# Kernel optimization log

Hardware: AMD Instinct MI355X
Metric: run time of the kernel (lower is better)

Reference implementation:

```python
import jax, jax.numpy as jnp
import numpy as np

EMBED_DIM = 768
N_HEADS = 12
HEAD_DIM = EMBED_DIM // N_HEADS


def setup_inputs() -> dict:
    key = jax.random.key(0)
    ks = jax.random.split(key, 6)
    bsz, seq = 2, 4096
    hidden_states = jax.random.normal(ks[0], (bsz, seq, EMBED_DIM), dtype=jnp.float32)
    attention_mask = jnp.zeros((bsz, 1, 1, seq), dtype=jnp.float32)
    s = 1.0 / np.sqrt(EMBED_DIM)
    Wq = jax.random.normal(ks[1], (EMBED_DIM, EMBED_DIM), dtype=jnp.float32) * s
    Wk = jax.random.normal(ks[2], (EMBED_DIM, EMBED_DIM), dtype=jnp.float32) * s
    Wv = jax.random.normal(ks[3], (EMBED_DIM, EMBED_DIM), dtype=jnp.float32) * s
    Wo = jax.random.normal(ks[4], (EMBED_DIM, EMBED_DIM), dtype=jnp.float32) * s
    bo = jax.random.normal(ks[5], (EMBED_DIM,), dtype=jnp.float32) * s
    return {"hidden_states": hidden_states, "attention_mask": attention_mask,
            "Wq": Wq, "Wk": Wk, "Wv": Wv, "Wo": Wo, "bo": bo}


def reference(hidden_states, attention_mask, Wq, Wk, Wv, Wo, bo):
    bsz, seq, _ = hidden_states.shape
    scale = 1.0 / np.sqrt(HEAD_DIM)

    def split_heads(x):  # [b, s, e] -> [b, h, s, d]
        return x.reshape(bsz, seq, N_HEADS, HEAD_DIM).transpose(0, 2, 1, 3)

    # nn.Linear applies x @ W.T
    q = split_heads(hidden_states @ Wq.T)
    k = split_heads(hidden_states @ Wk.T)
    v = split_heads(hidden_states @ Wv.T)

    # [b, h, tgt, src] score matrix (faithful to the bmm+softmax+bmm original)
    attn = jnp.einsum('bhqd,bhkd->bhqk', q, k) * scale
    attn = attn + attention_mask  # mask broadcasts [b,1,1,src]
    probs = jax.nn.softmax(attn, axis=-1)
    ctx = jnp.einsum('bhqk,bhkd->bhqd', probs, v)

    concat = ctx.transpose(0, 2, 1, 3).reshape(bsz, seq, EMBED_DIM)
    return concat @ Wo.T + bo
```

## Files before the change

kernel.cpp:

```cpp
#include <hip/hip_runtime.h>
#include <stdint.h>

#define ED   768
#define NH   12
#define HD   64
#define SEQ  4096
#define BSZ  2
#define BHT  (BSZ*NH)
#define MTOT (BSZ*SEQ)

typedef short bf16x8  __attribute__((ext_vector_type(8)));
typedef float f32x4   __attribute__((ext_vector_type(4)));
typedef float f32x16  __attribute__((ext_vector_type(16)));

#define LOG2E 1.44269504088896340736f
#define C2    (0.125f * LOG2E)

__device__ __forceinline__ unsigned short f2bf(float f) {
    union { float f; uint32_t u; } v; v.f = f;
    uint32_t u = v.u;
    u += 0x7fffu + ((u >> 16) & 1u);
    return (unsigned short)(u >> 16);
}

#if defined(__has_builtin)
#if __has_builtin(__builtin_amdgcn_cvt_pk_bf16_f32)
#define HAVE_CVT_PK_BF16 1
#endif
#endif
__device__ __forceinline__ uint32_t pkbf16(float a, float b) {
#ifdef HAVE_CVT_PK_BF16
    typedef __bf16 bf16x2_t __attribute__((ext_vector_type(2)));
    union { bf16x2_t v; uint32_t u; } c;
    c.v = __builtin_amdgcn_cvt_pk_bf16_f32(a, b);
    return c.u;
#else
    union { float f; uint32_t u; } x, y; x.f = a; y.f = b;
    return __builtin_amdgcn_perm(y.u + 0x8000u, x.u + 0x8000u, 0x07060302u);
#endif
}

__device__ __forceinline__ void cp16(const unsigned short* g, unsigned short* l) {
    __builtin_amdgcn_global_load_lds(
        (const __attribute__((address_space(1))) unsigned int*)(const void*)g,
        (__attribute__((address_space(3))) unsigned int*)(void*)l,
        16, 0, 0);
}

#define H_CHUNKS  (MTOT * ED / 4)
#define W_CHUNKS  (ED * ED / 4)
#define CVT_TOTAL (H_CHUNKS + 4 * W_CHUNKS)

__global__ __launch_bounds__(256) void convert_bf16(
    const float* __restrict__ H,  const float* __restrict__ Wq,
    const float* __restrict__ Wk, const float* __restrict__ Wv,
    const float* __restrict__ Wo, unsigned short* __restrict__ dst,
    unsigned short* __restrict__ WoB) {
    int i4 = blockIdx.x * 256 + threadIdx.x;
    float4 v;
    ushort4* optr;
    if (i4 < H_CHUNKS) { v = ((const float4*)H)[i4]; optr = (ushort4*)dst + i4; }
    else {
        int j = i4 - H_CHUNKS;
        if (j < 3 * W_CHUNKS) {
            if (j < W_CHUNKS)          v = ((const float4*)Wq)[j];
            else if (j < 2 * W_CHUNKS) v = ((const float4*)Wk)[j - W_CHUNKS];
            else                       v = ((const float4*)Wv)[j - 2 * W_CHUNKS];
            optr = (ushort4*)dst + i4;
        } else {
            v = ((const float4*)Wo)[j - 3 * W_CHUNKS];
            optr = (ushort4*)WoB + (j - 3 * W_CHUNKS);
        }
    }
    ushort4 o;
    o.x = f2bf(v.x); o.y = f2bf(v.y); o.z = f2bf(v.z); o.w = f2bf(v.w);
    *optr = o;
}

__global__ __launch_bounds__(256) void qkv_gemm(
    const unsigned short* __restrict__ Hb,
    const unsigned short* __restrict__ Wb,
    unsigned short* __restrict__ qkv) {
    __shared__ __align__(16) unsigned short Ah[128 * 64];
    __shared__ __align__(16) unsigned short Bh[128 * 64];
    const int t = threadIdx.x, w = t >> 6, lane = t & 63;
    const int quad = lane >> 4, r16 = lane & 15;
    const int wm = w >> 1, wn = w & 1;
    const int m0 = blockIdx.y * 128, n0g = blockIdx.x * 128;
    const int wsel = n0g / ED, n0 = n0g % ED;
    const int lrow = lane >> 3;
    const int lchs = ((lane & 7) ^ (lrow & 7)) * 8;

    f32x4 acc[4][4] = {};
    for (int kt = 0; kt < ED / 64; ++kt) {
        const int k0 = kt * 64;
#pragma unroll
        for (int i = 0; i < 4; ++i) {
            int row = i * 32 + w * 8;
            cp16(&Hb[(size_t)(m0 + row + lrow) * ED + k0 + lchs], &Ah[row * 64]);
            cp16(&Wb[(size_t)(n0g + row + lrow) * ED + k0 + lchs], &Bh[row * 64]);
        }
        __syncthreads();
#pragma unroll
        for (int kk = 0; kk < 2; ++kk) {
            bf16x8 aF[4], bF[4];
#pragma unroll
            for (int mi = 0; mi < 4; ++mi) {
                int R = wm * 64 + mi * 16 + r16;
                aF[mi] = *(const bf16x8*)&Ah[R * 64 + (((kk * 4 + quad) ^ (r16 & 7)) * 8)];
            }
#pragma unroll
            for (int ni = 0; ni < 4; ++ni) {
                int R = wn * 64 + ni * 16 + r16;
                bF[ni] = *(const bf16x8*)&Bh[R * 64 + (((kk * 4 + quad) ^ (r16 & 7)) * 8)];
            }
            if (wsel == 2) {
#pragma unroll
                for (int mi = 0; mi < 4; ++mi)
#pragma unroll
                    for (int ni = 0; ni < 4; ++ni)
                        acc[mi][ni] = __builtin_amdgcn_mfma_f32_16x16x32_bf16(
                            bF[ni], aF[mi], acc[mi][ni], 0, 0, 0);
            } else {
#pragma unroll
                for (int mi = 0; mi < 4; ++mi)
#pragma unroll
                    for (int ni = 0; ni < 4; ++ni)
                        acc[mi][ni] = __builtin_amdgcn_mfma_f32_16x16x32_bf16(
                            aF[mi], bF[ni], acc[mi][ni], 0, 0, 0);
            }
        }
        __syncthreads();
    }
    const size_t WSZ = (size_t)BHT * SEQ * HD;
    if (wsel == 2) {
#pragma unroll
        for (int mi = 0; mi < 4; ++mi)
#pragma unroll
            for (int ni = 0; ni < 4; ++ni)
#pragma unroll
                for (int r = 0; r < 4; ++r) {
                    int m  = m0 + wm * 64 + mi * 16 + r16;
                    int nn = n0 + wn * 64 + ni * 16 + quad * 4 + r;
                    int b = m >> 12, s = m & 4095;
                    int hh = nn >> 6, dd = nn & 63;
                    qkv[2 * WSZ + (((size_t)b * NH + hh) * HD + dd) * SEQ + s] =
                        f2bf(acc[mi][ni][r]);
                }
    } else {
        const float sc = (wsel == 0) ? C2 : 1.0f;
#pragma unroll
        for (int mi = 0; mi < 4; ++mi)
#pragma unroll
            for (int ni = 0; ni < 4; ++ni)
#pragma unroll
                for (int r = 0; r < 4; ++r) {
                    int m = m0 + wm * 64 + mi * 16 + quad * 4 + r;
                    int b = m >> 12, s = m & 4095;
                    int nn = n0 + wn * 64 + ni * 16 + r16;
                    int hh = nn >> 6, dd = nn & 63;
                    size_t off = (((size_t)b * NH + hh) * SEQ + s) * HD + dd;
                    qkv[(size_t)wsel * WSZ + off] = f2bf(acc[mi][ni][r] * sc);
                }
    }
}

__global__ __launch_bounds__(256) void flash_attn(
    const unsigned short* __restrict__ qkv, const float* __restrict__ mask,
    unsigned short* __restrict__ ctx) {
    __shared__ __align__(16) unsigned short Ksm[64 * 64];
    __shared__ __align__(16) unsigned short Vtsm[64 * 64];
    __shared__ __align__(16) unsigned short Psm[4][32][72];
    __shared__ unsigned short Msm[64];
    const int t  = threadIdx.x;
    const int bh = blockIdx.y;
    const int b  = bh / NH;
    const int h  = bh % NH;
    const int qbase = blockIdx.x * 128;
    const size_t WSZ = (size_t)BHT * SEQ * HD;
    const unsigned short* Qp = qkv + (size_t)bh * SEQ * HD;
    const unsigned short* Kp = Qp + WSZ;
    const unsigned short* Vt = qkv + 2 * WSZ + (size_t)bh * HD * SEQ;
    const int w = t >> 6, lane = t & 63, n31 = lane & 31, hi = lane >> 5;
    const int lrow = lane >> 3;
    const int lchs = ((lane & 7) ^ (lrow & 7)) * 8;
    const int sw = n31 & 7;

    bf16x8 qF[4];
    {
        int qrow = qbase + w * 32 + n31;
#pragma unroll
        for (int kc = 0; kc < 4; ++kc)
            qF[kc] = *(const bf16x8*)&Qp[(size_t)qrow * HD + kc * 16 + hi * 8];
    }
    bf16x8 bOnes = {};
    if (hi == 0) bOnes[0] = (short)0x3F80;
    bf16x8 aOnes;
#pragma unroll
    for (int j = 0; j < 8; ++j) aOnes[j] = (short)0x3F80;
    const f32x16 kZero = {};

    f32x16 oAcc[2] = {};
    f32x16 lAcc = {};

    for (int kt = 0; kt < SEQ / 64; ++kt) {
#pragma unroll
        for (int i = 0; i < 2; ++i) {
            int row = w * 16 + i * 8;
            cp16(&Kp[(size_t)(kt * 64 + row + lrow) * HD + lchs], &Ksm[row * 64]);
            cp16(&Vt[(size_t)(row + lrow) * SEQ + kt * 64 + lchs], &Vtsm[row * 64]);
        }
        if (t < 64) Msm[t] = f2bf(LOG2E * mask[b * SEQ + kt * 64 + t]);
        __syncthreads();

#pragma unroll
        for (int st = 0; st < 2; ++st) {
            bf16x8 am = {};
            {
                unsigned short mv = Msm[st * 32 + n31];
                am[0] = (hi == 0) ? (short)mv : (short)0;
            }
            f32x16 sA = __builtin_amdgcn_mfma_f32_32x32x16_bf16(am, bOnes, kZero, 0, 0, 0);
#pragma unroll
            for (int kc = 0; kc < 4; ++kc) {
                bf16x8 kF = *(const bf16x8*)
                    &Ksm[(st * 32 + n31) * 64 + (((2 * kc + hi) ^ sw) * 8)];
                sA = __builtin_amdgcn_mfma_f32_32x32x16_bf16(kF, qF[kc], sA, 0, 0, 0);
            }
#pragma unroll
            for (int g = 0; g < 4; ++g) {
                float p0 = __builtin_amdgcn_exp2f(sA[4 * g + 0]);
                float p1 = __builtin_amdgcn_exp2f(sA[4 * g + 1]);
                float p2 = __builtin_amdgcn_exp2f(sA[4 * g + 2]);
                float p3 = __builtin_amdgcn_exp2f(sA[4 * g + 3]);
                uint2 dd;
                dd.x = pkbf16(p0, p1);
                dd.y = pkbf16(p2, p3);
                *(uint2*)&Psm[w][n31][st * 32 + hi * 4 + 8 * g] = dd;
            }
        }

#pragma unroll
        for (int kc = 0; kc < 4; ++kc) {
            bf16x8 pF = *(const bf16x8*)&Psm[w][n31][kc * 16 + hi * 8];
            lAcc = __builtin_amdgcn_mfma_f32_32x32x16_bf16(aOnes, pF, lAcc, 0, 0, 0);
#pragma unroll
            for (int dt = 0; dt < 2; ++dt) {
                bf16x8 vF = *(const bf16x8*)
                    &Vtsm[(dt * 32 + n31) * 64 + (((2 * kc + hi) ^ sw) * 8)];
                oAcc[dt] = __builtin_amdgcn_mfma_f32_32x32x16_bf16(vF, pF, oAcc[dt], 0, 0, 0);
            }
        }
        __syncthreads();
    }
    float inv = 1.0f / lAcc[0];
    int s = qbase + w * 32 + n31;
    unsigned short* obase = &ctx[((size_t)b * SEQ + s) * ED + h * HD];
#pragma unroll
    for (int dt = 0; dt < 2; ++dt)
#pragma unroll
        for (int g = 0; g < 4; ++g) {
            uint2 o;
            o.x = pkbf16(oAcc[dt][4 * g + 0] * inv, oAcc[dt][4 * g + 1] * inv);
            o.y = pkbf16(oAcc[dt][4 * g + 2] * inv, oAcc[dt][4 * g + 3] * inv);
            *(uint2*)&obase[dt * 32 + hi * 4 + 8 * g] = o;
        }
}

__global__ __launch_bounds__(256) void out_gemm(
    const unsigned short* __restrict__ Ab,
    const unsigned short* __restrict__ Wob,
    const float* __restrict__ bo, float* __restrict__ out) {
    __shared__ __align__(16) unsigned short Ah[128 * 64];
    __shared__ __align__(16) unsigned short Bh[128 * 64];
    const int t = threadIdx.x, w = t >> 6, lane = t & 63;
    const int quad = lane >> 4, r16 = lane & 15;
    const int wm = w >> 1, wn = w & 1;
    const int m0 = blockIdx.y * 128, n0 = blockIdx.x * 128;
    const int lrow = lane >> 3;
    const int lchs = ((lane & 7) ^ (lrow & 7)) * 8;

    f32x4 acc[4][4] = {};
    for (int kt = 0; kt < ED / 64; ++kt) {
        const int k0 = kt * 64;
#pragma unroll
        for (int i = 0; i < 4; ++i) {
            int row = i * 32 + w * 8;
            cp16(&Ab[(size_t)(m0 + row + lrow) * ED + k0 + lchs], &Ah[row * 64]);
            cp16(&Wob[(size_t)(n0 + row + lrow) * ED + k0 + lchs], &Bh[row * 64]);
        }
        __syncthreads();
#pragma unroll
        for (int kk = 0; kk < 2; ++kk) {
            bf16x8 aF[4], bF[4];
#pragma unroll
            for (int mi = 0; mi < 4; ++mi) {
                int R = wm * 64 + mi * 16 + r16;
                aF[mi] = *(const bf16x8*)&Ah[R * 64 + (((kk * 4 + quad) ^ (r16 & 7)) * 8)];
            }
#pragma unroll
            for (int ni = 0; ni < 4; ++ni) {
                int R = wn * 64 + ni * 16 + r16;
                bF[ni] = *(const bf16x8*)&Bh[R * 64 + (((kk * 4 + quad) ^ (r16 & 7)) * 8)];
            }
#pragma unroll
            for (int mi = 0; mi < 4; ++mi)
#pragma unroll
                for (int ni = 0; ni < 4; ++ni)
                    acc[mi][ni] = __builtin_amdgcn_mfma_f32_16x16x32_bf16(
                        aF[mi], bF[ni], acc[mi][ni], 0, 0, 0);
        }
        __syncthreads();
    }
    float bov[4];
#pragma unroll
    for (int ni = 0; ni < 4; ++ni) bov[ni] = bo[n0 + wn * 64 + ni * 16 + r16];
#pragma unroll
    for (int mi = 0; mi < 4; ++mi)
#pragma unroll
        for (int ni = 0; ni < 4; ++ni)
#pragma unroll
            for (int r = 0; r < 4; ++r) {
                int m = m0 + wm * 64 + mi * 16 + quad * 4 + r;
                int n = n0 + wn * 64 + ni * 16 + r16;
                out[(size_t)m * ED + n] = acc[mi][ni][r] + bov[ni];
            }
}

extern "C" void kernel_launch(void* const* d_in, const int* in_sizes, int n_in,
                              void* d_out, int out_size, void* d_ws, size_t ws_size,
                              hipStream_t stream) {
    const float* H    = (const float*)d_in[0];
    const float* mask = (const float*)d_in[1];
    const float* Wq   = (const float*)d_in[2];
    const float* Wk   = (const float*)d_in[3];
    const float* Wv   = (const float*)d_in[4];
    const float* Wo   = (const float*)d_in[5];
    const float* bo   = (const float*)d_in[6];
    unsigned short* ws = (unsigned short*)d_ws;
    const size_t WSZ = (size_t)BHT * SEQ * HD;
    unsigned short* qkv = ws;
    unsigned short* ctx = ws + 3 * WSZ;
    unsigned short* WoB = ctx + (size_t)MTOT * ED;
    float* out = (float*)d_out;
    unsigned short* Hb = (unsigned short*)d_out;
    unsigned short* Wb = Hb + (size_t)MTOT * ED;

    convert_bf16<<<CVT_TOTAL / 256, 256, 0, stream>>>(H, Wq, Wk, Wv, Wo, Hb, WoB);
    qkv_gemm<<<dim3(3 * ED / 128, MTOT / 128), 256, 0, stream>>>(Hb, Wb, qkv);
    flash_attn<<<dim3(SEQ / 128, BHT), 256, 0, stream>>>(qkv, mask, ctx);
    out_gemm<<<dim3(ED / 128, MTOT / 128), 256, 0, stream>>>(ctx, WoB, bo, out);
}
```

Before: 343.4 us.

## Load K/V fragments directly from global memory, drop LDS staging and barriers

The flash attention kernel stops staging K and V tiles in shared memory. Each wave now reads its MFMA fragments straight from global memory, which removes both __syncthreads per tile. The mask is pre-converted to bf16 (scaled by log2e) in the convert kernel. The row-sum MFMA against a ones vector is replaced by scalar accumulation of the exp values plus a final cross-half shuffle. The trade is that the four waves now each fetch the same K/V data through L1/L2 with unswizzled, strided loads (V rows strided by SEQ), and loads are no longer shared or prefetched through LDS.

```diff
diff --git a/kernel.cpp b/kernel.cpp
--- a/kernel.cpp
+++ b/kernel.cpp
@@ -49,13 +49,15 @@
 
 #define H_CHUNKS  (MTOT * ED / 4)
 #define W_CHUNKS  (ED * ED / 4)
-#define CVT_TOTAL (H_CHUNKS + 4 * W_CHUNKS)
+#define MB_CHUNKS (BSZ * SEQ / 4)
+#define CVT_TOTAL (H_CHUNKS + 4 * W_CHUNKS + MB_CHUNKS)
 
 __global__ __launch_bounds__(256) void convert_bf16(
     const float* __restrict__ H,  const float* __restrict__ Wq,
     const float* __restrict__ Wk, const float* __restrict__ Wv,
-    const float* __restrict__ Wo, unsigned short* __restrict__ dst,
-    unsigned short* __restrict__ WoB) {
+    const float* __restrict__ Wo, const float* __restrict__ Mask,
+    unsigned short* __restrict__ dst, unsigned short* __restrict__ WoB,
+    unsigned short* __restrict__ maskB) {
     int i4 = blockIdx.x * 256 + threadIdx.x;
     float4 v;
     ushort4* optr;
@@ -67,9 +69,17 @@
             else if (j < 2 * W_CHUNKS) v = ((const float4*)Wk)[j - W_CHUNKS];
             else                       v = ((const float4*)Wv)[j - 2 * W_CHUNKS];
             optr = (ushort4*)dst + i4;
-        } else {
+        } else if (j < 4 * W_CHUNKS) {
             v = ((const float4*)Wo)[j - 3 * W_CHUNKS];
             optr = (ushort4*)WoB + (j - 3 * W_CHUNKS);
+        } else {
+            int m = j - 4 * W_CHUNKS;
+            float4 mv = ((const float4*)Mask)[m];
+            ushort4 o;
+            o.x = f2bf(LOG2E * mv.x); o.y = f2bf(LOG2E * mv.y);
+            o.z = f2bf(LOG2E * mv.z); o.w = f2bf(LOG2E * mv.w);
+            ((ushort4*)maskB)[m] = o;
+            return;
         }
     }
     ushort4 o;
@@ -166,12 +176,10 @@
 }
 
 __global__ __launch_bounds__(256) void flash_attn(
-    const unsigned short* __restrict__ qkv, const float* __restrict__ mask,
+    const unsigned short* __restrict__ qkv,
+    const unsigned short* __restrict__ maskB,
     unsigned short* __restrict__ ctx) {
-    __shared__ __align__(16) unsigned short Ksm[64 * 64];
-    __shared__ __align__(16) unsigned short Vtsm[64 * 64];
     __shared__ __align__(16) unsigned short Psm[4][32][72];
-    __shared__ unsigned short Msm[64];
     const int t  = threadIdx.x;
     const int bh = blockIdx.y;
     const int b  = bh / NH;
@@ -181,10 +189,8 @@
     const unsigned short* Qp = qkv + (size_t)bh * SEQ * HD;
     const unsigned short* Kp = Qp + WSZ;
     const unsigned short* Vt = qkv + 2 * WSZ + (size_t)bh * HD * SEQ;
+    const unsigned short* mrow = maskB + b * SEQ;
     const int w = t >> 6, lane = t & 63, n31 = lane & 31, hi = lane >> 5;
-    const int lrow = lane >> 3;
-    const int lchs = ((lane & 7) ^ (lrow & 7)) * 8;
-    const int sw = n31 & 7;
 
     bf16x8 qF[4];
     {
@@ -195,65 +201,58 @@
     }
     bf16x8 bOnes = {};
     if (hi == 0) bOnes[0] = (short)0x3F80;
-    bf16x8 aOnes;
-#pragma unroll
-    for (int j = 0; j < 8; ++j) aOnes[j] = (short)0x3F80;
     const f32x16 kZero = {};
 
     f32x16 oAcc[2] = {};
-    f32x16 lAcc = {};
+    float l_i = 0.0f;
 
     for (int kt = 0; kt < SEQ / 64; ++kt) {
-#pragma unroll
-        for (int i = 0; i < 2; ++i) {
-            int row = w * 16 + i * 8;
-            cp16(&Kp[(size_t)(kt * 64 + row + lrow) * HD + lchs], &Ksm[row * 64]);
-            cp16(&Vt[(size_t)(row + lrow) * SEQ + kt * 64 + lchs], &Vtsm[row * 64]);
-        }
-        if (t < 64) Msm[t] = f2bf(LOG2E * mask[b * SEQ + kt * 64 + t]);
-        __syncthreads();
+        const unsigned short* Kt = Kp + (size_t)kt * 64 * HD;
+        const unsigned short* Vk = Vt + kt * 64;
 
 #pragma unroll
         for (int st = 0; st < 2; ++st) {
             bf16x8 am = {};
             {
-                unsigned short mv = Msm[st * 32 + n31];
+                unsigned short mv = mrow[kt * 64 + st * 32 + n31];
                 am[0] = (hi == 0) ? (short)mv : (short)0;
             }
             f32x16 sA = __builtin_amdgcn_mfma_f32_32x32x16_bf16(am, bOnes, kZero, 0, 0, 0);
 #pragma unroll
             for (int kc = 0; kc < 4; ++kc) {
                 bf16x8 kF = *(const bf16x8*)
-                    &Ksm[(st * 32 + n31) * 64 + (((2 * kc + hi) ^ sw) * 8)];
+                    &Kt[(size_t)(st * 32 + n31) * HD + kc * 16 + hi * 8];
                 sA = __builtin_amdgcn_mfma_f32_32x32x16_bf16(kF, qF[kc], sA, 0, 0, 0);
             }
+            float r0 = 0.f, r1 = 0.f, r2 = 0.f, r3 = 0.f;
 #pragma unroll
             for (int g = 0; g < 4; ++g) {
                 float p0 = __builtin_amdgcn_exp2f(sA[4 * g + 0]);
                 float p1 = __builtin_amdgcn_exp2f(sA[4 * g + 1]);
                 float p2 = __builtin_amdgcn_exp2f(sA[4 * g + 2]);
                 float p3 = __builtin_amdgcn_exp2f(sA[4 * g + 3]);
+                r0 += p0; r1 += p1; r2 += p2; r3 += p3;
                 uint2 dd;
                 dd.x = pkbf16(p0, p1);
                 dd.y = pkbf16(p2, p3);
                 *(uint2*)&Psm[w][n31][st * 32 + hi * 4 + 8 * g] = dd;
             }
+            l_i += (r0 + r1) + (r2 + r3);
         }
 
 #pragma unroll
         for (int kc = 0; kc < 4; ++kc) {
             bf16x8 pF = *(const bf16x8*)&Psm[w][n31][kc * 16 + hi * 8];
-            lAcc = __builtin_amdgcn_mfma_f32_32x32x16_bf16(aOnes, pF, lAcc, 0, 0, 0);
 #pragma unroll
             for (int dt = 0; dt < 2; ++dt) {
                 bf16x8 vF = *(const bf16x8*)
-                    &Vtsm[(dt * 32 + n31) * 64 + (((2 * kc + hi) ^ sw) * 8)];
+                    &Vk[(size_t)(dt * 32 + n31) * SEQ + kc * 16 + hi * 8];
                 oAcc[dt] = __builtin_amdgcn_mfma_f32_32x32x16_bf16(vF, pF, oAcc[dt], 0, 0, 0);
             }
         }
-        __syncthreads();
-    }
-    float inv = 1.0f / lAcc[0];
+    }
+    l_i += __shfl_xor(l_i, 32);
+    float inv = 1.0f / l_i;
     int s = qbase + w * 32 + n31;
     unsigned short* obase = &ctx[((size_t)b * SEQ + s) * ED + h * HD];
 #pragma unroll
@@ -339,15 +338,17 @@
     const float* bo   = (const float*)d_in[6];
     unsigned short* ws = (unsigned short*)d_ws;
     const size_t WSZ = (size_t)BHT * SEQ * HD;
-    unsigned short* qkv = ws;
-    unsigned short* ctx = ws + 3 * WSZ;
-    unsigned short* WoB = ctx + (size_t)MTOT * ED;
+    unsigned short* qkv   = ws;
+    unsigned short* ctx   = ws + 3 * WSZ;
+    unsigned short* WoB   = ctx + (size_t)MTOT * ED;
+    unsigned short* maskB = WoB + (size_t)ED * ED;
     float* out = (float*)d_out;
     unsigned short* Hb = (unsigned short*)d_out;
     unsigned short* Wb = Hb + (size_t)MTOT * ED;
 
-    convert_bf16<<<CVT_TOTAL / 256, 256, 0, stream>>>(H, Wq, Wk, Wv, Wo, Hb, WoB);
+    convert_bf16<<<CVT_TOTAL / 256, 256, 0, stream>>>(H, Wq, Wk, Wv, Wo, mask,
+                                                      Hb, WoB, maskB);
     qkv_gemm<<<dim3(3 * ED / 128, MTOT / 128), 256, 0, stream>>>(Hb, Wb, qkv);
-    flash_attn<<<dim3(SEQ / 128, BHT), 256, 0, stream>>>(qkv, mask, ctx);
+    flash_attn<<<dim3(SEQ / 128, BHT), 256, 0, stream>>>(qkv, maskB, ctx);
     out_gemm<<<dim3(ED / 128, MTOT / 128), 256, 0, stream>>>(ctx, WoB, bo, out);
 }
```

Result: slower. 498.9 us (+45.3%).
